# Performance work log

Measured on AMD Instinct MI355X. Metric: run time of the kernel, lower is better.

The kernel has to match this reference:

```python
import jax, jax.numpy as jnp
import numpy as np

DIM, K_RANK, L, N_CLASS = 64, 16, 8, 10
H = 1e-3
B = 256
DD = DIM * DIM  # 4096


def _cay(C, D):
    # Cayley transform of B = C @ D^T : I + C (I - 0.5 D^T C)^{-1} D^T
    Id = jnp.eye(C.shape[1], dtype=C.dtype)
    DT = jnp.swapaxes(D, 1, 2)
    inv = jnp.linalg.inv(Id - 0.5 * DT @ C)
    return Id + C @ inv @ DT


def setup_inputs() -> dict:
    key = jax.random.key(0)
    ks = jax.random.split(key, 9)
    u = jax.random.normal(ks[0], (B, DIM, K_RANK), jnp.float32) / np.float32(np.sqrt(DIM))
    vh = jax.random.normal(ks[1], (B, K_RANK, DIM), jnp.float32) / np.float32(np.sqrt(DIM))
    eye_k = jnp.eye(K_RANK, dtype=jnp.float32)
    off = 0.05 * jax.random.normal(ks[2], (B, K_RANK, K_RANK), jnp.float32) * (1.0 - eye_k)
    dvals = jax.random.uniform(ks[3], (B, K_RANK), jnp.float32, 0.5, 1.5)
    s_core = off + dvals[:, :, None] * eye_k  # diag bounded away from 0 (invert_S)
    s_block = jnp.zeros((B, DIM, K_RANK), jnp.float32).at[:, :K_RANK, :K_RANK].set(s_core)
    X = jnp.stack([u.reshape(B, -1), s_block.reshape(B, -1), vh.reshape(B, -1)], axis=1)
    sc = np.float32(1.0 / np.sqrt(DD))
    W0 = sc * jax.random.normal(ks[4], (DD, DD), jnp.float32)
    W = sc * jax.random.normal(ks[5], (L, DD, DD), jnp.float32)
    b = sc * jax.random.normal(ks[6], (L, DD), jnp.float32)
    Wc = sc * jax.random.normal(ks[7], (N_CLASS, DD), jnp.float32)
    bc = sc * jax.random.normal(ks[8], (N_CLASS,), jnp.float32)
    return {"X": X, "W0": W0, "W": W, "b": b, "Wc": Wc, "bc": bc}


def reference(X, W0, W, b, Wc, bc):
    Bn = X.shape[0]
    u = X[:, 0].reshape(Bn, DIM, K_RANK)
    s = X[:, 1].reshape(Bn, DIM, K_RANK)[:, :K_RANK, :K_RANK]
    vh = X[:, 2].reshape(Bn, K_RANK, DIM)
    v = jnp.swapaxes(vh, 1, 2)
    eye_k = jnp.eye(K_RANK, dtype=X.dtype)
    eye_d = jnp.eye(DIM, dtype=X.dtype)
    Xf = (u @ s @ vh).reshape(Bn, DD)
    outs = []
    for i in range(L + 1):  # layer 0 has no bias
        lin = Xf @ W0.T if i == 0 else Xf @ W[i - 1].T + b[i - 1]
        dY = jax.nn.relu(lin).reshape(Bn, DIM, DIM)
        # invert_S: invert only the diagonal of s
        s_inv = (1.0 / jnp.diagonal(s, axis1=1, axis2=2))[:, :, None] * eye_k
        dU = dY @ v @ s_inv
        dV = jnp.swapaxes(dY, 1, 2) @ u @ jnp.swapaxes(s_inv, 1, 2)
        dS = jnp.swapaxes(u, 1, 2) @ dY @ v
        uT = jnp.swapaxes(u, 1, 2)
        F = (eye_d - u @ uT) @ dU
        FT = jnp.swapaxes(F, 1, 2)
        u = _cay(H * (F @ uT), -H * (u @ FT)) @ u
        vT = jnp.swapaxes(v, 1, 2)
        F = (eye_d - v @ vT) @ dV
        FT = jnp.swapaxes(F, 1, 2)
        v = _cay(H * (F @ vT), -H * (v @ FT)) @ v
        s = s + H * dS
        Xf = (u @ s @ jnp.swapaxes(v, 1, 2)).reshape(Bn, DD)
        outs.append(Xf)
    X_transformed = jnp.stack(outs, axis=-1)  # (B, dim*dim, L+1)
    X_classified = Xf @ Wc.T + bc
    X_predicted = jax.nn.softmax(X_classified, axis=1)
    return X_predicted, X_classified, X_transformed
```

## Files before the change

### kernel.cpp

```cpp
#include <hip/hip_runtime.h>
#include <math.h>

typedef unsigned short u16;
typedef unsigned int u32;
using bf16x8 = __attribute__((ext_vector_type(8))) short;
using f32x4  = __attribute__((ext_vector_type(4))) float;

#define DD 4096
#define NB 256
#define SPLIT_K 4
#define PSTRIDE (NB * DD)
#define PLANE (NB * DD)

__device__ __forceinline__ u16 f2bf(float f) {
  unsigned int u = __float_as_uint(f);
  u += 0x7fffu + ((u >> 16) & 1u);
  return (u16)(u >> 16);
}
__device__ __forceinline__ float bf2f(u16 h) {
  return __uint_as_float((u32)h << 16);
}
__device__ __forceinline__ unsigned int pack2bf(float a, float b) {
  return (unsigned int)f2bf(a) | ((unsigned int)f2bf(b) << 16);
}
__device__ __forceinline__ void async_cp16(const u16* g, u16* l) {
  __builtin_amdgcn_global_load_lds(
      (const __attribute__((address_space(1))) unsigned int*)g,
      (__attribute__((address_space(3))) unsigned int*)l, 16, 0, 0);
}

__global__ __launch_bounds__(512, 8) void gemm_kernel(
    const u16* __restrict__ A, const float* __restrict__ W,
    u16* __restrict__ part)
{
  const int nt = blockIdx.x;
  const int mt = blockIdx.y & 1;
  const int kz = blockIdx.y >> 1;
  const int t = threadIdx.x;
  const int w = t >> 6, l = t & 63;

  __shared__ __align__(16) u16 As[128 * 64];
  __shared__ __align__(16) u16 Bs[64 * 64];

  const int colg0 = nt << 6;
  const int m0 = mt << 7;
  const int k0 = kz << 10;

  f32x4 acc[2][2];
#pragma unroll
  for (int mi = 0; mi < 2; ++mi)
#pragma unroll
    for (int nj = 0; nj < 2; ++nj)
      acc[mi][nj] = (f32x4){0.f, 0.f, 0.f, 0.f};

  const int wm = w & 3, wn = w >> 2;
  const int lr = l & 15, lg = l >> 4;
  const int arow_l = (w << 3) + (l >> 3);
  const int acl = l & 7;
  const int bn_l = t >> 3;
  const int bcc = t & 7;

  for (int tt = 0; tt < 16; ++tt) {
    const int kk = k0 + (tt << 6);
    __syncthreads();
#pragma unroll
    for (int r2 = 0; r2 < 2; ++r2) {
      const int row = (r2 << 6) + arow_l;
      const int cs = acl ^ (row & 7);
      async_cp16(A + ((size_t)(m0 + row) << 12) + kk + (cs << 3),
                 &As[(r2 << 12) + (w << 9)]);
    }
    {
      const float* wsrc = W + ((size_t)(colg0 + bn_l) << 12) + kk + (bcc << 3);
      const float4 f0 = *reinterpret_cast<const float4*>(wsrc);
      const float4 f1 = *reinterpret_cast<const float4*>(wsrc + 4);
      uint4 pk;
      pk.x = pack2bf(f0.x, f0.y);
      pk.y = pack2bf(f0.z, f0.w);
      pk.z = pack2bf(f1.x, f1.y);
      pk.w = pack2bf(f1.z, f1.w);
      *reinterpret_cast<uint4*>(&Bs[(bn_l << 6) + ((bcc ^ (bn_l & 7)) << 3)]) = pk;
    }
    __syncthreads();
#pragma unroll
    for (int ks = 0; ks < 2; ++ks) {
      const int cg = (ks << 2) + lg;
      bf16x8 av[2], bv[2];
#pragma unroll
      for (int mi = 0; mi < 2; ++mi) {
        const int fr = (wm << 5) + (mi << 4) + lr;
        av[mi] = *reinterpret_cast<const bf16x8*>(&As[(fr << 6) + ((cg ^ (fr & 7)) << 3)]);
      }
#pragma unroll
      for (int nj = 0; nj < 2; ++nj) {
        const int fc = (wn << 5) + (nj << 4) + lr;
        bv[nj] = *reinterpret_cast<const bf16x8*>(&Bs[(fc << 6) + ((cg ^ (fc & 7)) << 3)]);
      }
#pragma unroll
      for (int mi = 0; mi < 2; ++mi)
#pragma unroll
        for (int nj = 0; nj < 2; ++nj)
          acc[mi][nj] = __builtin_amdgcn_mfma_f32_16x16x32_bf16(
              av[mi], bv[nj], acc[mi][nj], 0, 0, 0);
    }
  }

  u16* pout = part + (size_t)kz * PSTRIDE;
#pragma unroll
  for (int mi = 0; mi < 2; ++mi)
#pragma unroll
    for (int nj = 0; nj < 2; ++nj) {
      const int col = colg0 + (wn << 5) + (nj << 4) + lr;
#pragma unroll
      for (int j = 0; j < 4; ++j) {
        const int row = m0 + (wm << 5) + (mi << 4) + (lg << 2) + j;
        pout[((size_t)row << 12) + col] = f2bf(acc[mi][nj][j]);
      }
    }
}

struct UpdSmem {
  float U[64][17], V[64][17], P[64][17], Q[64][17];
  float S[16][16];
  float sinv[16];
  union {
    struct {
      float dY[64][68];
      float dYT[64][69];
    };
    struct {
      float Fu[64][17], Fv[64][17];
      float R[16][17], Rv[16][17];
      float G1u[16][17], G1v[16][17];
      float G2u[16][17], G2v[16][17];
      float M1u[16][17], M1v[16][17];
    };
  };
};

__device__ __forceinline__ void write_xf_tail(
    UpdSmem& m, int t, int b, float* __restrict__ Xf, u16* __restrict__ Xfb,
    float* __restrict__ outL_plane)
{
  const int p = t >> 3;
  const int j0 = (t << 1) & 15;
  {
    float a0 = 0.f, a1 = 0.f;
    for (int k = 0; k < 16; ++k) {
      const float uk = m.U[p][k];
      a0 += uk * m.S[k][j0];
      a1 += uk * m.S[k][j0 + 1];
    }
    m.P[p][j0] = a0; m.P[p][j0 + 1] = a1;
  }
  __syncthreads();
  {
    const int q0 = (t & 7) << 3;
    float res[8];
#pragma unroll
    for (int e = 0; e < 8; ++e) res[e] = 0.f;
    for (int i = 0; i < 16; ++i) {
      const float pi = m.P[p][i];
#pragma unroll
      for (int e = 0; e < 8; ++e) res[e] += pi * m.V[q0 + e][i];
    }
    const size_t ko = ((size_t)b << 12) + (p << 6) + q0;
    float4* xo = reinterpret_cast<float4*>(Xf + ko);
    const float4 r0 = make_float4(res[0], res[1], res[2], res[3]);
    const float4 r1 = make_float4(res[4], res[5], res[6], res[7]);
    xo[0] = r0; xo[1] = r1;
    uint4 pk;
    pk.x = pack2bf(res[0], res[1]); pk.y = pack2bf(res[2], res[3]);
    pk.z = pack2bf(res[4], res[5]); pk.w = pack2bf(res[6], res[7]);
    *reinterpret_cast<uint4*>(Xfb + ko) = pk;
    if (outL_plane != nullptr) {
      float4* op = reinterpret_cast<float4*>(outL_plane + ko);
      op[0] = r0; op[1] = r1;
    }
  }
}

__global__ __launch_bounds__(512) void update_kernel(
    const u16* __restrict__ part, const float* __restrict__ bias,
    float* __restrict__ u_g, float* __restrict__ v_g, float* __restrict__ s_g,
    float* __restrict__ Xf, u16* __restrict__ Xfb,
    float* __restrict__ outL, int layer)
{
  const int b = blockIdx.x, t = threadIdx.x;
  __shared__ __align__(16) UpdSmem m;
  float* outL_plane = outL + (size_t)layer * PLANE;
  const size_t ub = (size_t)b << 10;
  const int p = t >> 3;
  const int j0 = (t << 1) & 15;

  {
    const float2 u2 = *reinterpret_cast<const float2*>(u_g + ub + (t << 1));
    const float2 v2 = *reinterpret_cast<const float2*>(v_g + ub + (t << 1));
    const int r = t >> 3, c = (t & 7) << 1;
    m.U[r][c] = u2.x; m.U[r][c + 1] = u2.y;
    m.V[r][c] = v2.x; m.V[r][c + 1] = v2.y;
    if (t < 256) m.S[t >> 4][t & 15] = s_g[((size_t)b << 8) + t];
    if (t < 16)  m.sinv[t] = 1.0f / s_g[((size_t)b << 8) + t * 17];
    const u16* p0 = part + ((size_t)b << 12) + (t << 3);
    float x[8];
#pragma unroll
    for (int e = 0; e < 8; ++e) x[e] = 0.f;
#pragma unroll
    for (int kzi = 0; kzi < SPLIT_K; ++kzi) {
      const uint4 v = *reinterpret_cast<const uint4*>(p0 + (size_t)kzi * PSTRIDE);
      x[0] += bf2f((u16)(v.x & 0xffff)); x[1] += bf2f((u16)(v.x >> 16));
      x[2] += bf2f((u16)(v.y & 0xffff)); x[3] += bf2f((u16)(v.y >> 16));
      x[4] += bf2f((u16)(v.z & 0xffff)); x[5] += bf2f((u16)(v.z >> 16));
      x[6] += bf2f((u16)(v.w & 0xffff)); x[7] += bf2f((u16)(v.w >> 16));
    }
    if (bias != nullptr) {
      const float4 b0 = *reinterpret_cast<const float4*>(bias + (t << 3));
      const float4 b1 = *reinterpret_cast<const float4*>(bias + (t << 3) + 4);
      x[0] += b0.x; x[1] += b0.y; x[2] += b0.z; x[3] += b0.w;
      x[4] += b1.x; x[5] += b1.y; x[6] += b1.z; x[7] += b1.w;
    }
    const int r2 = t >> 3, c2 = (t & 7) << 3;
#pragma unroll
    for (int e = 0; e < 8; ++e) x[e] = fmaxf(x[e], 0.f);
    float4* d0 = reinterpret_cast<float4*>(&m.dY[r2][c2]);
    d0[0] = make_float4(x[0], x[1], x[2], x[3]);
    d0[1] = make_float4(x[4], x[5], x[6], x[7]);
#pragma unroll
    for (int e = 0; e < 8; ++e) m.dYT[c2 + e][r2] = x[e];
  }
  __syncthreads();

  {
    float a0 = 0.f, a1 = 0.f;
    for (int q = 0; q < 64; ++q) {
      const float d = m.dY[p][q];
      a0 += d * m.V[q][j0];
      a1 += d * m.V[q][j0 + 1];
    }
    float b0 = 0.f, b1 = 0.f;
    for (int r = 0; r < 64; ++r) {
      const float d = m.dYT[p][r];
      b0 += d * m.U[r][j0];
      b1 += d * m.U[r][j0 + 1];
    }
    m.P[p][j0] = a0; m.P[p][j0 + 1] = a1;
    m.Q[p][j0] = b0; m.Q[p][j0 + 1] = b1;
  }
  __syncthreads();

  {
    const int i = (t >> 4) & 15, j = t & 15;
    if (t < 256) {
      float r0 = 0.f, g0 = 0.f;
      for (int r = 0; r < 64; ++r) {
        const float ui = m.U[r][i];
        r0 += ui * m.P[r][j];
        g0 += ui * m.U[r][j];
      }
      m.R[i][j] = r0; m.G2u[i][j] = g0;
    } else {
      float r0 = 0.f, g0 = 0.f;
      for (int r = 0; r < 64; ++r) {
        const float vi = m.V[r][i];
        r0 += vi * m.Q[r][j];
        g0 += vi * m.V[r][j];
      }
      m.Rv[i][j] = r0; m.G2v[i][j] = g0;
    }
  }
  __syncthreads();

  {
    float f0 = m.P[p][j0], f1 = m.P[p][j0 + 1];
    float g0 = m.Q[p][j0], g1 = m.Q[p][j0 + 1];
    for (int k = 0; k < 16; ++k) {
      const float uk = m.U[p][k], vk = m.V[p][k];
      f0 -= uk * m.R[k][j0];
      f1 -= uk * m.R[k][j0 + 1];
      g0 -= vk * m.Rv[k][j0];
      g1 -= vk * m.Rv[k][j0 + 1];
    }
    const float s0 = m.sinv[j0], s1 = m.sinv[j0 + 1];
    m.Fu[p][j0] = f0 * s0; m.Fu[p][j0 + 1] = f1 * s1;
    m.Fv[p][j0] = g0 * s0; m.Fv[p][j0 + 1] = g1 * s1;
  }
  __syncthreads();

  {
    const int i = (t >> 4) & 15, j = t & 15;
    if (t < 256) {
      float g = 0.f;
      for (int r = 0; r < 64; ++r) g += m.U[r][i] * m.Fu[r][j];
      m.G1u[i][j] = g;
    } else {
      float g = 0.f;
      for (int r = 0; r < 64; ++r) g += m.V[r][i] * m.Fv[r][j];
      m.G1v[i][j] = g;
    }
  }
  __syncthreads();

  {
    const int i = (t >> 4) & 15, j = t & 15;
    if (t < 256) {
      float mm = 0.f;
      for (int k = 0; k < 16; ++k) mm += m.G1u[i][k] * m.G2u[k][j];
      m.M1u[i][j] = mm;
    } else {
      float mm = 0.f;
      for (int k = 0; k < 16; ++k) mm += m.G1v[i][k] * m.G2v[k][j];
      m.M1v[i][j] = mm;
    }
  }
  __syncthreads();

  {
    float du0 = 0.f, du1 = 0.f, dv0 = 0.f, dv1 = 0.f;
    for (int k = 0; k < 16; ++k) {
      const float fu = m.Fu[p][k], fv = m.Fv[p][k];
      du0 += fu * m.M1u[k][j0];
      du1 += fu * m.M1u[k][j0 + 1];
      dv0 += fv * m.M1v[k][j0];
      dv1 += fv * m.M1v[k][j0 + 1];
    }
    const float nu0 = m.U[p][j0]     - 1e-6f * du0;
    const float nu1 = m.U[p][j0 + 1] - 1e-6f * du1;
    const float nv0 = m.V[p][j0]     - 1e-6f * dv0;
    const float nv1 = m.V[p][j0 + 1] - 1e-6f * dv1;
    float ns = 0.f;
    if (t < 256) {
      const int i = t >> 4, j = t & 15;
      ns = m.S[i][j] + 1e-3f * m.R[i][j];
    }
    __syncthreads();
    m.U[p][j0] = nu0; m.U[p][j0 + 1] = nu1;
    m.V[p][j0] = nv0; m.V[p][j0 + 1] = nv1;
    *reinterpret_cast<float2*>(u_g + ub + (p << 4) + j0) = make_float2(nu0, nu1);
    *reinterpret_cast<float2*>(v_g + ub + (p << 4) + j0) = make_float2(nv0, nv1);
    if (t < 256) {
      const int i = t >> 4, j = t & 15;
      m.S[i][j] = ns;
      s_g[((size_t)b << 8) + t] = ns;
    }
  }
  __syncthreads();

  write_xf_tail(m, t, b, Xf, Xfb, outL_plane);
}

__global__ __launch_bounds__(512) void init_kernel(
    const float* __restrict__ X, float* __restrict__ u_g, float* __restrict__ v_g,
    float* __restrict__ s_g, float* __restrict__ Xf, u16* __restrict__ Xfb)
{
  const int b = blockIdx.x, t = threadIdx.x;
  __shared__ __align__(16) UpdSmem m;
  const float* xb = X + (size_t)b * 3072;
  const size_t ub = (size_t)b << 10;
  {
    const float2 u2 = *reinterpret_cast<const float2*>(xb + (t << 1));
    const int r = t >> 3, c = (t & 7) << 1;
    m.U[r][c] = u2.x; m.U[r][c + 1] = u2.y;
    *reinterpret_cast<float2*>(u_g + ub + (t << 1)) = u2;
    if (t < 256) {
      const float sv = xb[1024 + t];
      m.S[t >> 4][t & 15] = sv;
      s_g[((size_t)b << 8) + t] = sv;
    }
    const float2 v2 = *reinterpret_cast<const float2*>(xb + 2048 + (t << 1));
    const int g2 = t << 1;
    const int iv = g2 >> 6, q = g2 & 63;
    m.V[q][iv] = v2.x; m.V[q + 1][iv] = v2.y;
    v_g[ub + (size_t)q * 16 + iv] = v2.x;
    v_g[ub + (size_t)(q + 1) * 16 + iv] = v2.y;
  }
  __syncthreads();
  write_xf_tail(m, t, b, Xf, Xfb, nullptr);
}

__global__ __launch_bounds__(256) void pack_kernel(
    const float* __restrict__ outL, float* __restrict__ outT)
{
  const int t = threadIdx.x;
  const int base = blockIdx.x << 8;
  __shared__ float buf[256 * 9];
#pragma unroll
  for (int l = 0; l < 9; ++l)
    buf[t * 9 + l] = outL[(size_t)l * PLANE + base + t];
  __syncthreads();
  const float4* b4 = reinterpret_cast<const float4*>(buf);
  float4* o4 = reinterpret_cast<float4*>(outT + (size_t)base * 9);
  for (int i = t; i < 576; i += 256) o4[i] = b4[i];
}

__global__ __launch_bounds__(256) void classifier_kernel(
    const float* __restrict__ Xf, const float* __restrict__ Wc,
    const float* __restrict__ bc, float* __restrict__ pred, float* __restrict__ cls)
{
  const int b = blockIdx.x, t = threadIdx.x;
  const int lane = t & 63, w = t >> 6;
  __shared__ float red[4][10];
  float acc[10];
#pragma unroll
  for (int c = 0; c < 10; ++c) acc[c] = 0.f;
  const float* xr = Xf + ((size_t)b << 12);
  for (int k = t; k < 4096; k += 256) {
    const float x = xr[k];
#pragma unroll
    for (int c = 0; c < 10; ++c) acc[c] += x * Wc[c * 4096 + k];
  }
#pragma unroll
  for (int c = 0; c < 10; ++c)
    for (int off = 32; off; off >>= 1) acc[c] += __shfl_xor(acc[c], off);
  if (lane == 0)
#pragma unroll
    for (int c = 0; c < 10; ++c) red[w][c] = acc[c];
  __syncthreads();
  if (t == 0) {
    float lg[10], ex[10];
    float m = -1e30f;
#pragma unroll
    for (int c = 0; c < 10; ++c) {
      lg[c] = red[0][c] + red[1][c] + red[2][c] + red[3][c] + bc[c];
      m = fmaxf(m, lg[c]);
    }
    float s = 0.f;
#pragma unroll
    for (int c = 0; c < 10; ++c) { ex[c] = expf(lg[c] - m); s += ex[c]; }
    const float inv = 1.f / s;
#pragma unroll
    for (int c = 0; c < 10; ++c) {
      cls[b * 10 + c] = lg[c];
      pred[b * 10 + c] = ex[c] * inv;
    }
  }
}

extern "C" void kernel_launch(void* const* d_in, const int* in_sizes, int n_in,
                              void* d_out, int out_size, void* d_ws, size_t ws_size,
                              hipStream_t stream) {
  (void)in_sizes; (void)n_in; (void)out_size; (void)ws_size;
  const float* X  = (const float*)d_in[0];
  const float* W0 = (const float*)d_in[1];
  const float* W  = (const float*)d_in[2];
  const float* bb = (const float*)d_in[3];
  const float* Wc = (const float*)d_in[4];
  const float* bc = (const float*)d_in[5];

  float* out_pred  = (float*)d_out;
  float* out_cls   = out_pred + 2560;
  float* out_trans = out_pred + 5120;

  char* ws = (char*)d_ws;
  float* Xf   = (float*)(ws);
  u16*   part = (u16*)  (ws + (4ull << 20));
  float* u_g  = (float*)(ws + (36ull << 20));
  float* v_g  = (float*)(ws + (37ull << 20));
  float* s_g  = (float*)(ws + (38ull << 20));
  u16*   Xfb  = (u16*)  (ws + (39ull << 20));
  float* outL = (float*)(ws + (41ull << 20));

  init_kernel<<<NB, 512, 0, stream>>>(X, u_g, v_g, s_g, Xf, Xfb);
  for (int i = 0; i <= 8; ++i) {
    const float* Wl = (i == 0) ? W0 : W + (size_t)(i - 1) * DD * DD;
    gemm_kernel<<<dim3(64, 2 * SPLIT_K), 512, 0, stream>>>(Xfb, Wl, part);
    update_kernel<<<NB, 512, 0, stream>>>(
        part, (i == 0) ? nullptr : (bb + (size_t)(i - 1) * DD),
        u_g, v_g, s_g, Xf, Xfb, outL, i);
  }
  pack_kernel<<<4096, 256, 0, stream>>>(outL, out_trans);
  classifier_kernel<<<NB, 256, 0, stream>>>(Xf, Wc, bc, out_pred, out_cls);
}
```

Measured before the change: 420.1 us.

## Store update-kernel operands as transposed bf16 rows and vectorize small matmuls

Rewrites the per-sample update kernel so dY, U, V, P, Q and F are kept in shared memory as transposed bf16 rows. Inner products then run as 128-bit vector loads with dot8 helpers, and the 16x16 products use float4 dots over transposed copies (ST, RT, M1T). The pack and classifier kernels are fused into one launch. The aim is to cut LDS instruction count and bank conflicts in the latency-bound update kernel, at the cost of bf16 rounding in the intermediate dY products.

```diff
diff --git a/kernel.cpp b/kernel.cpp
--- a/kernel.cpp
+++ b/kernel.cpp
@@ -27,6 +27,21 @@
   __builtin_amdgcn_global_load_lds(
       (const __attribute__((address_space(1))) unsigned int*)g,
       (__attribute__((address_space(3))) unsigned int*)l, 16, 0, 0);
+}
+__device__ __forceinline__ float dot8bf(const uint4 a, const uint4 b) {
+  float s;
+  s  = __uint_as_float(a.x << 16) * __uint_as_float(b.x << 16);
+  s += __uint_as_float(a.x & 0xffff0000u) * __uint_as_float(b.x & 0xffff0000u);
+  s += __uint_as_float(a.y << 16) * __uint_as_float(b.y << 16);
+  s += __uint_as_float(a.y & 0xffff0000u) * __uint_as_float(b.y & 0xffff0000u);
+  s += __uint_as_float(a.z << 16) * __uint_as_float(b.z << 16);
+  s += __uint_as_float(a.z & 0xffff0000u) * __uint_as_float(b.z & 0xffff0000u);
+  s += __uint_as_float(a.w << 16) * __uint_as_float(b.w << 16);
+  s += __uint_as_float(a.w & 0xffff0000u) * __uint_as_float(b.w & 0xffff0000u);
+  return s;
+}
+__device__ __forceinline__ float dot4f(const float4 a, const float4 b) {
+  return a.x * b.x + a.y * b.y + a.z * b.z + a.w * b.w;
 }
 
 __global__ __launch_bounds__(512, 8) void gemm_kernel(
@@ -120,20 +135,22 @@
 }
 
 struct UpdSmem {
-  float U[64][17], V[64][17], P[64][17], Q[64][17];
-  float S[16][16];
+  float U[64][20], V[64][20], P[64][20];
+  u16 UTb[16][72], VTb[16][72], PTb[16][72], QTb[16][72];
+  float S[16][16], ST[16][16];
   float sinv[16];
   union {
     struct {
-      float dY[64][68];
-      float dYT[64][69];
+      u16 dYb[64][72];
+      u16 dYTb[64][80];
     };
     struct {
-      float Fu[64][17], Fv[64][17];
-      float R[16][17], Rv[16][17];
-      float G1u[16][17], G1v[16][17];
-      float G2u[16][17], G2v[16][17];
-      float M1u[16][17], M1v[16][17];
+      float Fu[64][20], Fv[64][20];
+      u16 FuTb[16][72], FvTb[16][72];
+      float R[16][20], RT[16][20], RvT[16][20];
+      float G1u[16][20], G1v[16][20];
+      float G2u[16][20], G2v[16][20];
+      float M1uT[16][20], M1vT[16][20];
     };
   };
 };
@@ -145,24 +162,31 @@
   const int p = t >> 3;
   const int j0 = (t << 1) & 15;
   {
+    const float4* u4 = reinterpret_cast<const float4*>(&m.U[p][0]);
+    const float4* sa = reinterpret_cast<const float4*>(&m.ST[j0][0]);
+    const float4* sb = reinterpret_cast<const float4*>(&m.ST[j0 + 1][0]);
     float a0 = 0.f, a1 = 0.f;
-    for (int k = 0; k < 16; ++k) {
-      const float uk = m.U[p][k];
-      a0 += uk * m.S[k][j0];
-      a1 += uk * m.S[k][j0 + 1];
+#pragma unroll
+    for (int k4 = 0; k4 < 4; ++k4) {
+      const float4 uu = u4[k4];
+      a0 += dot4f(uu, sa[k4]);
+      a1 += dot4f(uu, sb[k4]);
     }
     m.P[p][j0] = a0; m.P[p][j0 + 1] = a1;
   }
   __syncthreads();
   {
     const int q0 = (t & 7) << 3;
+    float4 pr[4];
+    const float4* p4 = reinterpret_cast<const float4*>(&m.P[p][0]);
+#pragma unroll
+    for (int k4 = 0; k4 < 4; ++k4) pr[k4] = p4[k4];
     float res[8];
 #pragma unroll
-    for (int e = 0; e < 8; ++e) res[e] = 0.f;
-    for (int i = 0; i < 16; ++i) {
-      const float pi = m.P[p][i];
-#pragma unroll
-      for (int e = 0; e < 8; ++e) res[e] += pi * m.V[q0 + e][i];
+    for (int e = 0; e < 8; ++e) {
+      const float4* v4 = reinterpret_cast<const float4*>(&m.V[q0 + e][0]);
+      res[e] = dot4f(pr[0], v4[0]) + dot4f(pr[1], v4[1]) +
+               dot4f(pr[2], v4[2]) + dot4f(pr[3], v4[3]);
     }
     const size_t ko = ((size_t)b << 12) + (p << 6) + q0;
     float4* xo = reinterpret_cast<float4*>(Xf + ko);
@@ -190,7 +214,7 @@
   __shared__ __align__(16) UpdSmem m;
   float* outL_plane = outL + (size_t)layer * PLANE;
   const size_t ub = (size_t)b << 10;
-  const int p = t >> 3;
+  const int p8 = t >> 3;
   const int j0 = (t << 1) & 15;
 
   {
@@ -199,8 +223,14 @@
     const int r = t >> 3, c = (t & 7) << 1;
     m.U[r][c] = u2.x; m.U[r][c + 1] = u2.y;
     m.V[r][c] = v2.x; m.V[r][c + 1] = v2.y;
-    if (t < 256) m.S[t >> 4][t & 15] = s_g[((size_t)b << 8) + t];
-    if (t < 16)  m.sinv[t] = 1.0f / s_g[((size_t)b << 8) + t * 17];
+    m.UTb[c][r] = f2bf(u2.x); m.UTb[c + 1][r] = f2bf(u2.y);
+    m.VTb[c][r] = f2bf(v2.x); m.VTb[c + 1][r] = f2bf(v2.y);
+    if (t < 256) {
+      const float sv = s_g[((size_t)b << 8) + t];
+      m.S[t >> 4][t & 15] = sv;
+      m.ST[t & 15][t >> 4] = sv;
+    }
+    if (t < 16) m.sinv[t] = 1.0f / s_g[((size_t)b << 8) + t * 17];
     const u16* p0 = part + ((size_t)b << 12) + (t << 3);
     float x[8];
 #pragma unroll
@@ -219,127 +249,169 @@
       x[0] += b0.x; x[1] += b0.y; x[2] += b0.z; x[3] += b0.w;
       x[4] += b1.x; x[5] += b1.y; x[6] += b1.z; x[7] += b1.w;
     }
-    const int r2 = t >> 3, c2 = (t & 7) << 3;
 #pragma unroll
     for (int e = 0; e < 8; ++e) x[e] = fmaxf(x[e], 0.f);
-    float4* d0 = reinterpret_cast<float4*>(&m.dY[r2][c2]);
-    d0[0] = make_float4(x[0], x[1], x[2], x[3]);
-    d0[1] = make_float4(x[4], x[5], x[6], x[7]);
-#pragma unroll
-    for (int e = 0; e < 8; ++e) m.dYT[c2 + e][r2] = x[e];
-  }
-  __syncthreads();
-
-  {
-    float a0 = 0.f, a1 = 0.f;
-    for (int q = 0; q < 64; ++q) {
-      const float d = m.dY[p][q];
-      a0 += d * m.V[q][j0];
-      a1 += d * m.V[q][j0 + 1];
-    }
-    float b0 = 0.f, b1 = 0.f;
-    for (int r = 0; r < 64; ++r) {
-      const float d = m.dYT[p][r];
-      b0 += d * m.U[r][j0];
-      b1 += d * m.U[r][j0 + 1];
-    }
-    m.P[p][j0] = a0; m.P[p][j0 + 1] = a1;
-    m.Q[p][j0] = b0; m.Q[p][j0 + 1] = b1;
-  }
-  __syncthreads();
-
-  {
-    const int i = (t >> 4) & 15, j = t & 15;
+    const int r2 = t >> 3, c2 = (t & 7) << 3, sw = (t & 7) << 3;
+    uint4 pk;
+    pk.x = pack2bf(x[0], x[1]); pk.y = pack2bf(x[2], x[3]);
+    pk.z = pack2bf(x[4], x[5]); pk.w = pack2bf(x[6], x[7]);
+    *reinterpret_cast<uint4*>(&m.dYb[r2][c2]) = pk;
+#pragma unroll
+    for (int e = 0; e < 8; ++e) m.dYTb[c2 + e][r2 ^ sw] = f2bf(x[e]);
+  }
+  __syncthreads();
+
+  {
+    const int tt = t & 255;
+    const int p = tt & 63, jg = (tt >> 6) << 2;
+    float a[4] = {0.f, 0.f, 0.f, 0.f};
+    if (t < 256) {
+      const uint4* dy = reinterpret_cast<const uint4*>(&m.dYb[p][0]);
+#pragma unroll
+      for (int r8 = 0; r8 < 8; ++r8) {
+        const uint4 d = dy[r8];
+#pragma unroll
+        for (int e = 0; e < 4; ++e)
+          a[e] += dot8bf(d, reinterpret_cast<const uint4*>(&m.VTb[jg + e][0])[r8]);
+      }
+#pragma unroll
+      for (int e = 0; e < 4; ++e) m.PTb[jg + e][p] = f2bf(a[e]);
+    } else {
+      const int sw = (p >> 3) & 7;
+      const uint4* dy = reinterpret_cast<const uint4*>(&m.dYTb[p][0]);
+#pragma unroll
+      for (int r8 = 0; r8 < 8; ++r8) {
+        const uint4 d = dy[r8 ^ sw];
+#pragma unroll
+        for (int e = 0; e < 4; ++e)
+          a[e] += dot8bf(d, reinterpret_cast<const uint4*>(&m.UTb[jg + e][0])[r8]);
+      }
+#pragma unroll
+      for (int e = 0; e < 4; ++e) m.QTb[jg + e][p] = f2bf(a[e]);
+    }
+  }
+  __syncthreads();
+
+  {
+    const int tt = t & 255, i = tt >> 4, j = tt & 15;
     if (t < 256) {
       float r0 = 0.f, g0 = 0.f;
-      for (int r = 0; r < 64; ++r) {
-        const float ui = m.U[r][i];
-        r0 += ui * m.P[r][j];
-        g0 += ui * m.U[r][j];
-      }
-      m.R[i][j] = r0; m.G2u[i][j] = g0;
+#pragma unroll
+      for (int r8 = 0; r8 < 8; ++r8) {
+        const uint4 ui = reinterpret_cast<const uint4*>(&m.UTb[i][0])[r8];
+        r0 += dot8bf(ui, reinterpret_cast<const uint4*>(&m.PTb[j][0])[r8]);
+        g0 += dot8bf(ui, reinterpret_cast<const uint4*>(&m.UTb[j][0])[r8]);
+      }
+      m.R[i][j] = r0; m.RT[j][i] = r0; m.G2u[i][j] = g0;
     } else {
       float r0 = 0.f, g0 = 0.f;
-      for (int r = 0; r < 64; ++r) {
-        const float vi = m.V[r][i];
-        r0 += vi * m.Q[r][j];
-        g0 += vi * m.V[r][j];
-      }
-      m.Rv[i][j] = r0; m.G2v[i][j] = g0;
-    }
-  }
-  __syncthreads();
-
-  {
-    float f0 = m.P[p][j0], f1 = m.P[p][j0 + 1];
-    float g0 = m.Q[p][j0], g1 = m.Q[p][j0 + 1];
-    for (int k = 0; k < 16; ++k) {
-      const float uk = m.U[p][k], vk = m.V[p][k];
-      f0 -= uk * m.R[k][j0];
-      f1 -= uk * m.R[k][j0 + 1];
-      g0 -= vk * m.Rv[k][j0];
-      g1 -= vk * m.Rv[k][j0 + 1];
+#pragma unroll
+      for (int r8 = 0; r8 < 8; ++r8) {
+        const uint4 vi = reinterpret_cast<const uint4*>(&m.VTb[i][0])[r8];
+        r0 += dot8bf(vi, reinterpret_cast<const uint4*>(&m.QTb[j][0])[r8]);
+        g0 += dot8bf(vi, reinterpret_cast<const uint4*>(&m.VTb[j][0])[r8]);
+      }
+      m.RvT[j][i] = r0; m.G2v[i][j] = g0;
+    }
+  }
+  __syncthreads();
+
+  {
+    float f0 = bf2f(m.PTb[j0][p8]), f1 = bf2f(m.PTb[j0 + 1][p8]);
+    float g0 = bf2f(m.QTb[j0][p8]), g1 = bf2f(m.QTb[j0 + 1][p8]);
+    const float4* u4 = reinterpret_cast<const float4*>(&m.U[p8][0]);
+    const float4* v4 = reinterpret_cast<const float4*>(&m.V[p8][0]);
+    const float4* ra = reinterpret_cast<const float4*>(&m.RT[j0][0]);
+    const float4* rb = reinterpret_cast<const float4*>(&m.RT[j0 + 1][0]);
+    const float4* rc = reinterpret_cast<const float4*>(&m.RvT[j0][0]);
+    const float4* rd = reinterpret_cast<const float4*>(&m.RvT[j0 + 1][0]);
+#pragma unroll
+    for (int k4 = 0; k4 < 4; ++k4) {
+      const float4 uu = u4[k4], vv = v4[k4];
+      f0 -= dot4f(uu, ra[k4]);
+      f1 -= dot4f(uu, rb[k4]);
+      g0 -= dot4f(vv, rc[k4]);
+      g1 -= dot4f(vv, rd[k4]);
     }
     const float s0 = m.sinv[j0], s1 = m.sinv[j0 + 1];
-    m.Fu[p][j0] = f0 * s0; m.Fu[p][j0 + 1] = f1 * s1;
-    m.Fv[p][j0] = g0 * s0; m.Fv[p][j0 + 1] = g1 * s1;
-  }
-  __syncthreads();
-
-  {
-    const int i = (t >> 4) & 15, j = t & 15;
+    f0 *= s0; f1 *= s1; g0 *= s0; g1 *= s1;
+    *reinterpret_cast<float2*>(&m.Fu[p8][j0]) = make_float2(f0, f1);
+    *reinterpret_cast<float2*>(&m.Fv[p8][j0]) = make_float2(g0, g1);
+    m.FuTb[j0][p8] = f2bf(f0); m.FuTb[j0 + 1][p8] = f2bf(f1);
+    m.FvTb[j0][p8] = f2bf(g0); m.FvTb[j0 + 1][p8] = f2bf(g1);
+  }
+  __syncthreads();
+
+  {
+    const int tt = t & 255, i = tt >> 4, j = tt & 15;
     if (t < 256) {
       float g = 0.f;
-      for (int r = 0; r < 64; ++r) g += m.U[r][i] * m.Fu[r][j];
+#pragma unroll
+      for (int r8 = 0; r8 < 8; ++r8)
+        g += dot8bf(reinterpret_cast<const uint4*>(&m.UTb[i][0])[r8],
+                    reinterpret_cast<const uint4*>(&m.FuTb[j][0])[r8]);
       m.G1u[i][j] = g;
     } else {
       float g = 0.f;
-      for (int r = 0; r < 64; ++r) g += m.V[r][i] * m.Fv[r][j];
+#pragma unroll
+      for (int r8 = 0; r8 < 8; ++r8)
+        g += dot8bf(reinterpret_cast<const uint4*>(&m.VTb[i][0])[r8],
+                    reinterpret_cast<const uint4*>(&m.FvTb[j][0])[r8]);
       m.G1v[i][j] = g;
     }
   }
   __syncthreads();
 
   {
-    const int i = (t >> 4) & 15, j = t & 15;
+    const int tt = t & 255, i = tt >> 4, j = tt & 15;
     if (t < 256) {
       float mm = 0.f;
-      for (int k = 0; k < 16; ++k) mm += m.G1u[i][k] * m.G2u[k][j];
-      m.M1u[i][j] = mm;
+#pragma unroll
+      for (int k4 = 0; k4 < 4; ++k4)
+        mm += dot4f(reinterpret_cast<const float4*>(&m.G1u[i][0])[k4],
+                    reinterpret_cast<const float4*>(&m.G2u[j][0])[k4]);
+      m.M1uT[j][i] = mm;
     } else {
       float mm = 0.f;
-      for (int k = 0; k < 16; ++k) mm += m.G1v[i][k] * m.G2v[k][j];
-      m.M1v[i][j] = mm;
+#pragma unroll
+      for (int k4 = 0; k4 < 4; ++k4)
+        mm += dot4f(reinterpret_cast<const float4*>(&m.G1v[i][0])[k4],
+                    reinterpret_cast<const float4*>(&m.G2v[j][0])[k4]);
+      m.M1vT[j][i] = mm;
     }
   }
   __syncthreads();
 
   {
     float du0 = 0.f, du1 = 0.f, dv0 = 0.f, dv1 = 0.f;
-    for (int k = 0; k < 16; ++k) {
-      const float fu = m.Fu[p][k], fv = m.Fv[p][k];
-      du0 += fu * m.M1u[k][j0];
-      du1 += fu * m.M1u[k][j0 + 1];
-      dv0 += fv * m.M1v[k][j0];
-      dv1 += fv * m.M1v[k][j0 + 1];
-    }
-    const float nu0 = m.U[p][j0]     - 1e-6f * du0;
-    const float nu1 = m.U[p][j0 + 1] - 1e-6f * du1;
-    const float nv0 = m.V[p][j0]     - 1e-6f * dv0;
-    const float nv1 = m.V[p][j0 + 1] - 1e-6f * dv1;
+    const float4* fu4 = reinterpret_cast<const float4*>(&m.Fu[p8][0]);
+    const float4* fv4 = reinterpret_cast<const float4*>(&m.Fv[p8][0]);
+    const float4* ma = reinterpret_cast<const float4*>(&m.M1uT[j0][0]);
+    const float4* mb = reinterpret_cast<const float4*>(&m.M1uT[j0 + 1][0]);
+    const float4* mc = reinterpret_cast<const float4*>(&m.M1vT[j0][0]);
+    const float4* md = reinterpret_cast<const float4*>(&m.M1vT[j0 + 1][0]);
+#pragma unroll
+    for (int k4 = 0; k4 < 4; ++k4) {
+      const float4 fu = fu4[k4], fv = fv4[k4];
+      du0 += dot4f(fu, ma[k4]);
+      du1 += dot4f(fu, mb[k4]);
+      dv0 += dot4f(fv, mc[k4]);
+      dv1 += dot4f(fv, md[k4]);
+    }
+    const float nu0 = m.U[p8][j0]     - 1e-6f * du0;
+    const float nu1 = m.U[p8][j0 + 1] - 1e-6f * du1;
+    const float nv0 = m.V[p8][j0]     - 1e-6f * dv0;
+    const float nv1 = m.V[p8][j0 + 1] - 1e-6f * dv1;
     float ns = 0.f;
-    if (t < 256) {
-      const int i = t >> 4, j = t & 15;
-      ns = m.S[i][j] + 1e-3f * m.R[i][j];
-    }
+    if (t < 256) ns = m.S[t >> 4][t & 15] + 1e-3f * m.R[t >> 4][t & 15];
     __syncthreads();
-    m.U[p][j0] = nu0; m.U[p][j0 + 1] = nu1;
-    m.V[p][j0] = nv0; m.V[p][j0 + 1] = nv1;
-    *reinterpret_cast<float2*>(u_g + ub + (p << 4) + j0) = make_float2(nu0, nu1);
-    *reinterpret_cast<float2*>(v_g + ub + (p << 4) + j0) = make_float2(nv0, nv1);
-    if (t < 256) {
-      const int i = t >> 4, j = t & 15;
-      m.S[i][j] = ns;
+    m.U[p8][j0] = nu0; m.U[p8][j0 + 1] = nu1;
+    m.V[p8][j0] = nv0; m.V[p8][j0 + 1] = nv1;
+    *reinterpret_cast<float2*>(u_g + ub + (p8 << 4) + j0) = make_float2(nu0, nu1);
+    *reinterpret_cast<float2*>(v_g + ub + (p8 << 4) + j0) = make_float2(nv0, nv1);
+    if (t < 256) {
+      m.S[t >> 4][t & 15] = ns;
+      m.ST[t & 15][t >> 4] = ns;
       s_g[((size_t)b << 8) + t] = ns;
     }
   }
@@ -364,6 +436,7 @@
     if (t < 256) {
       const float sv = xb[1024 + t];
       m.S[t >> 4][t & 15] = sv;
+      m.ST[t & 15][t >> 4] = sv;
       s_g[((size_t)b << 8) + t] = sv;
     }
     const float2 v2 = *reinterpret_cast<const float2*>(xb + 2048 + (t << 1));
@@ -377,28 +450,29 @@
   write_xf_tail(m, t, b, Xf, Xfb, nullptr);
 }
 
-__global__ __launch_bounds__(256) void pack_kernel(
-    const float* __restrict__ outL, float* __restrict__ outT)
+__global__ __launch_bounds__(256) void pack_cls_kernel(
+    const float* __restrict__ outL, float* __restrict__ outT,
+    const float* __restrict__ Xf, const float* __restrict__ Wc,
+    const float* __restrict__ bc, float* __restrict__ pred,
+    float* __restrict__ cls)
 {
   const int t = threadIdx.x;
-  const int base = blockIdx.x << 8;
+  const int bid = blockIdx.x;
   __shared__ float buf[256 * 9];
-#pragma unroll
-  for (int l = 0; l < 9; ++l)
-    buf[t * 9 + l] = outL[(size_t)l * PLANE + base + t];
-  __syncthreads();
-  const float4* b4 = reinterpret_cast<const float4*>(buf);
-  float4* o4 = reinterpret_cast<float4*>(outT + (size_t)base * 9);
-  for (int i = t; i < 576; i += 256) o4[i] = b4[i];
-}
-
-__global__ __launch_bounds__(256) void classifier_kernel(
-    const float* __restrict__ Xf, const float* __restrict__ Wc,
-    const float* __restrict__ bc, float* __restrict__ pred, float* __restrict__ cls)
-{
-  const int b = blockIdx.x, t = threadIdx.x;
+  __shared__ float red[4][10];
+  {
+    const int base = bid << 8;
+#pragma unroll
+    for (int l = 0; l < 9; ++l)
+      buf[t * 9 + l] = outL[(size_t)l * PLANE + base + t];
+    __syncthreads();
+    const float4* b4 = reinterpret_cast<const float4*>(buf);
+    float4* o4 = reinterpret_cast<float4*>(outT + (size_t)base * 9);
+    for (int i = t; i < 576; i += 256) o4[i] = b4[i];
+  }
+  if (bid >= NB) return;
+  const int b = bid;
   const int lane = t & 63, w = t >> 6;
-  __shared__ float red[4][10];
   float acc[10];
 #pragma unroll
   for (int c = 0; c < 10; ++c) acc[c] = 0.f;
@@ -417,15 +491,15 @@
   __syncthreads();
   if (t == 0) {
     float lg[10], ex[10];
-    float m = -1e30f;
+    float mx = -1e30f;
 #pragma unroll
     for (int c = 0; c < 10; ++c) {
       lg[c] = red[0][c] + red[1][c] + red[2][c] + red[3][c] + bc[c];
-      m = fmaxf(m, lg[c]);
+      mx = fmaxf(mx, lg[c]);
     }
     float s = 0.f;
 #pragma unroll
-    for (int c = 0; c < 10; ++c) { ex[c] = expf(lg[c] - m); s += ex[c]; }
+    for (int c = 0; c < 10; ++c) { ex[c] = expf(lg[c] - mx); s += ex[c]; }
     const float inv = 1.f / s;
 #pragma unroll
     for (int c = 0; c < 10; ++c) {
@@ -467,6 +541,6 @@
         part, (i == 0) ? nullptr : (bb + (size_t)(i - 1) * DD),
         u_g, v_g, s_g, Xf, Xfb, outL, i);
   }
-  pack_kernel<<<4096, 256, 0, stream>>>(outL, out_trans);
-  classifier_kernel<<<NB, 256, 0, stream>>>(Xf, Wc, bc, out_pred, out_cls);
-}
+  pack_cls_kernel<<<4096, 256, 0, stream>>>(outL, out_trans, Xf, Wc, bc,
+                                            out_pred, out_cls);
+}
```

New measurement: 402.3 us. 4.2% less time.
